# Kernel tuning notes

Measured on AMD Instinct MI355X. Metric: run time of the kernel, lower is better.

The kernel has to match this reference:

```python
import jax, jax.numpy as jnp
import numpy as np

NSEG = 64          # static number of segments (labels in [0, NSEG))
MARGIN = 0.25
W_PUSH = 1.0
W_PULL = 0.1


def setup_inputs() -> dict:
    key = jax.random.key(0)
    k1, k2 = jax.random.split(key)
    preds = jax.random.normal(k1, (4, 2, 16, 512, 512), dtype=jnp.float32)
    labels = jax.random.randint(k2, (4, 1, 512, 512), 0, NSEG, dtype=jnp.int32)
    return {"preds": preds, "labels": labels}


def reference(preds, labels):
    B, S, D, H, W = preds.shape
    P = H * W
    tags = preds.reshape(B, S, D, P)      # [B, n_stack, tag_dim, P]
    seg = labels.reshape(B, P)            # [B, P]
    iu, ju = jnp.triu_indices(NSEG, k=1)  # static upper-triangular pairs

    def per_item(t, s):
        # t: [S, D, P], s: [P]
        # --- scatter-mean: per-segment centroids ---
        tt = t.reshape(S * D, P).T                               # [P, S*D]
        sums = jax.ops.segment_sum(tt, s, num_segments=NSEG)     # [NSEG, S*D]
        counts = jax.ops.segment_sum(jnp.ones((P,), t.dtype), s, num_segments=NSEG)
        cent = (sums / jnp.maximum(counts, 1.0)[:, None]).reshape(NSEG, S, D)
        c = jnp.transpose(cent, (1, 2, 0))                       # [S, D, NSEG]
        # --- push: pairwise L1-mean centroid distance, upper triangle ---
        dist = jnp.abs(c[:, :, :, None] - c[:, :, None, :]).mean(axis=1)  # [S, NSEG, NSEG]
        cd = dist[:, iu, ju]                                     # [S, NSEG*(NSEG-1)/2]
        push = jnp.mean(jax.nn.relu(MARGIN - cd) ** 2)
        # --- pull: gather centroids back to pixels ---
        pc = c[:, :, s]                                          # [S, D, P]
        d = jnp.abs(t - pc).mean(axis=1)                         # [S, P]
        pull = jnp.mean(d ** 2)
        return push, pull

    pushes, pulls = jax.vmap(per_item)(tags, seg)                # [B], [B]
    return (W_PUSH * pushes + W_PULL * pulls).mean()
```

## Files before the change

kernel.cpp:

```cpp
#include <hip/hip_runtime.h>
#include <hip/hip_bf16.h>

#define BB 4
#define SS 2
#define DD 16
#define CH 32
#define PP (512*512)
#define NSEGC 64
#define MARGINF 0.25f
#define CHUNK 1024
#define NCHUNK (PP/CHUNK)

typedef __attribute__((ext_vector_type(4))) float  f32x4;
typedef __attribute__((ext_vector_type(8))) short  short8;

__device__ inline short f2bf(float x) {
    union { __hip_bfloat16 h; short s; } u;
    u.h = __float2bfloat16(x);
    return u.s;
}

__global__ __launch_bounds__(256) void k_sums(const float* __restrict__ preds,
                                              const int* __restrict__ labels,
                                              float* __restrict__ g_sums,
                                              float* __restrict__ g_counts)
{
    __shared__ int   labs[CHUNK];
    __shared__ float buf[4][CH][68];
    __shared__ float cbuf[4][NSEGC];

    const int b    = blockIdx.x / NCHUNK;
    const int base = (blockIdx.x % NCHUNK) * CHUNK;
    const int tid  = threadIdx.x;
    const int w    = tid >> 6;
    const int l    = tid & 63;
    const int lm   = l & 15;
    const int lk   = l >> 4;

    ((int4*)labs)[tid] = ((const int4*)(labels + (size_t)b * PP + base))[tid];

    f32x4 acc[4][2];
    f32x4 accc[4];
#pragma unroll
    for (int mt = 0; mt < 4; ++mt) {
        accc[mt] = f32x4{0.f, 0.f, 0.f, 0.f};
#pragma unroll
        for (int nt = 0; nt < 2; ++nt) acc[mt][nt] = f32x4{0.f, 0.f, 0.f, 0.f};
    }
    short8 ones;
#pragma unroll
    for (int j = 0; j < 8; ++j) ones[j] = (short)0x3F80;

    __syncthreads();

    const float* pb = preds + (size_t)b * CH * PP + base;

#pragma unroll 2
    for (int c = 0; c < 8; ++c) {
        const int kbase = (w * 8 + c) * 32 + lk * 8;
        const int4 L0 = *(const int4*)&labs[kbase];
        const int4 L1 = *(const int4*)&labs[kbase + 4];
        const int labv[8] = {L0.x, L0.y, L0.z, L0.w, L1.x, L1.y, L1.z, L1.w};

        short8 af[4];
#pragma unroll
        for (int mt = 0; mt < 4; ++mt) {
            const int target = mt * 16 + lm;
#pragma unroll
            for (int j = 0; j < 8; ++j)
                af[mt][j] = (labv[j] == target) ? (short)0x3F80 : (short)0;
        }

#pragma unroll
        for (int nt = 0; nt < 2; ++nt) {
            const float* src = pb + (size_t)(nt * 16 + lm) * PP + kbase;
            const float4 v0 = ((const float4*)src)[0];
            const float4 v1 = ((const float4*)src)[1];
            short8 bf;
            bf[0] = f2bf(v0.x); bf[1] = f2bf(v0.y); bf[2] = f2bf(v0.z); bf[3] = f2bf(v0.w);
            bf[4] = f2bf(v1.x); bf[5] = f2bf(v1.y); bf[6] = f2bf(v1.z); bf[7] = f2bf(v1.w);
#pragma unroll
            for (int mt = 0; mt < 4; ++mt)
                acc[mt][nt] = __builtin_amdgcn_mfma_f32_16x16x32_bf16(af[mt], bf, acc[mt][nt], 0, 0, 0);
        }
#pragma unroll
        for (int mt = 0; mt < 4; ++mt)
            accc[mt] = __builtin_amdgcn_mfma_f32_16x16x32_bf16(af[mt], ones, accc[mt], 0, 0, 0);
    }

#pragma unroll
    for (int mt = 0; mt < 4; ++mt) {
#pragma unroll
        for (int nt = 0; nt < 2; ++nt)
            *(f32x4*)&buf[w][nt * 16 + lm][mt * 16 + lk * 4] = acc[mt][nt];
        if (lm == 0)
            *(f32x4*)&cbuf[w][mt * 16 + lk * 4] = accc[mt];
    }
    __syncthreads();

    for (int i = tid; i < CH * NSEGC; i += 256) {
        const int col = i >> 6, row = i & 63;
        const float s = buf[0][col][row] + buf[1][col][row] + buf[2][col][row] + buf[3][col][row];
        atomicAdd(&g_sums[(size_t)b * CH * NSEGC + i], s);
    }
    if (tid < NSEGC)
        atomicAdd(&g_counts[b * NSEGC + tid],
                  cbuf[0][tid] + cbuf[1][tid] + cbuf[2][tid] + cbuf[3][tid]);
}

__global__ __launch_bounds__(256) void k_push(const float* __restrict__ g_sums,
                                              const float* __restrict__ g_counts,
                                              float* __restrict__ g_cent,
                                              float* __restrict__ g_push)
{
    __shared__ float centB[CH * NSEGC];
    __shared__ float red[4];
    const int b = blockIdx.x;
    const int tid = threadIdx.x;

    for (int i = tid; i < CH * NSEGC; i += 256) {
        const int ch = i >> 6, seg = i & 63;
        const float cnt = fmaxf(g_counts[b * NSEGC + seg], 1.0f);
        const float c = g_sums[(size_t)b * CH * NSEGC + i] / cnt;
        centB[i] = c;
        g_cent[(size_t)b * NSEGC * CH + seg * CH + ch] = c;
    }
    __syncthreads();

    float acc = 0.f;
    for (int t = tid; t < SS * 2016; t += 256) {
        const int s = t / 2016;
        int rem = t % 2016;
        int i = 0;
        while (rem >= 63 - i) { rem -= 63 - i; ++i; }
        const int j = i + 1 + rem;
        float dsum = 0.f;
#pragma unroll
        for (int d = 0; d < DD; ++d) {
            const int ch = s * DD + d;
            dsum += fabsf(centB[ch * NSEGC + i] - centB[ch * NSEGC + j]);
        }
        const float cd = dsum * (1.f / DD);
        const float r = fmaxf(MARGINF - cd, 0.f);
        acc += r * r;
    }
    for (int o = 32; o > 0; o >>= 1) acc += __shfl_down(acc, o, 64);
    if ((tid & 63) == 0) red[tid >> 6] = acc;
    __syncthreads();
    if (tid == 0)
        g_push[b] = (red[0] + red[1] + red[2] + red[3]) * (1.0f / (SS * 2016));
}

__global__ __launch_bounds__(256) void k_pull(const float* __restrict__ preds,
                                              const int* __restrict__ labels,
                                              const float* __restrict__ g_cent,
                                              float* __restrict__ g_pull)
{
    __shared__ float centL[NSEGC * 33];
    __shared__ float red[4];
    const int b    = blockIdx.x / NCHUNK;
    const int base = (blockIdx.x % NCHUNK) * CHUNK;
    const int tid  = threadIdx.x;

    for (int i = tid; i < NSEGC * CH; i += 256) {
        const int seg = i >> 5, ch = i & 31;
        centL[seg * 33 + ch] = g_cent[(size_t)b * NSEGC * CH + i];
    }
    const int4 lv = ((const int4*)(labels + (size_t)b * PP + base))[tid];
    const int c0 = lv.x * 33, c1 = lv.y * 33, c2 = lv.z * 33, c3 = lv.w * 33;
    __syncthreads();

    const float* pb = preds + (size_t)b * CH * PP + base;
    float total = 0.f;
#pragma unroll
    for (int s = 0; s < SS; ++s) {
        float a0 = 0.f, a1 = 0.f, a2 = 0.f, a3 = 0.f;
#pragma unroll 8
        for (int d = 0; d < DD; ++d) {
            const int ch = s * DD + d;
            const float4 v = ((const float4*)(pb + (size_t)ch * PP))[tid];
            a0 += fabsf(v.x - centL[c0 + ch]);
            a1 += fabsf(v.y - centL[c1 + ch]);
            a2 += fabsf(v.z - centL[c2 + ch]);
            a3 += fabsf(v.w - centL[c3 + ch]);
        }
        float q;
        q = a0 * (1.f / DD); total += q * q;
        q = a1 * (1.f / DD); total += q * q;
        q = a2 * (1.f / DD); total += q * q;
        q = a3 * (1.f / DD); total += q * q;
    }
    for (int o = 32; o > 0; o >>= 1) total += __shfl_down(total, o, 64);
    if ((tid & 63) == 0) red[tid >> 6] = total;
    __syncthreads();
    if (tid == 0)
        atomicAdd(&g_pull[b], red[0] + red[1] + red[2] + red[3]);
}

__global__ void k_final(const float* __restrict__ g_push,
                        const float* __restrict__ g_pull,
                        float* __restrict__ out)
{
    if (threadIdx.x == 0 && blockIdx.x == 0) {
        float acc = 0.f;
        for (int b = 0; b < BB; ++b)
            acc += g_push[b] + 0.1f * (g_pull[b] * (1.0f / (SS * PP)));
        out[0] = acc * (1.0f / BB);
    }
}

extern "C" void kernel_launch(void* const* d_in, const int* in_sizes, int n_in,
                              void* d_out, int out_size, void* d_ws, size_t ws_size,
                              hipStream_t stream) {
    const float* preds  = (const float*)d_in[0];
    const int*   labels = (const int*)d_in[1];

    float* ws       = (float*)d_ws;
    float* g_sums   = ws;
    float* g_counts = g_sums + BB * CH * NSEGC;
    float* g_pull   = g_counts + BB * NSEGC;
    float* g_push   = g_pull + BB;
    float* g_cent   = g_push + BB;

    hipMemsetAsync(d_ws, 0, (size_t)(BB * CH * NSEGC + BB * NSEGC + BB) * sizeof(float), stream);

    k_sums <<<BB * NCHUNK, 256, 0, stream>>>(preds, labels, g_sums, g_counts);
    k_push <<<BB, 256, 0, stream>>>(g_sums, g_counts, g_cent, g_push);
    k_pull <<<BB * NCHUNK, 256, 0, stream>>>(preds, labels, g_cent, g_pull);
    k_final<<<1, 64, 0, stream>>>(g_push, g_pull, (float*)d_out);
}
```

Baseline: 92.08 us.

## Fuse push and final reduction into pull kernel with last-block finalize

Removes the separate push and final kernels. Each pull block now computes centroids directly from the sums and counts. The first chunk block of each batch also computes the push term, and the last block to finish, detected with an atomic done counter, writes the final scalar. This saves two kernel launches and the serial single-block push kernel. In exchange, every pull block repeats the centroid division, and the push work sits on one block per batch, which may stretch the tail.

Result: slower. 102.2 us (+11.0%).

```diff
diff --git a/kernel.cpp b/kernel.cpp
--- a/kernel.cpp
+++ b/kernel.cpp
@@ -108,55 +108,17 @@
                   cbuf[0][tid] + cbuf[1][tid] + cbuf[2][tid] + cbuf[3][tid]);
 }
 
-__global__ __launch_bounds__(256) void k_push(const float* __restrict__ g_sums,
-                                              const float* __restrict__ g_counts,
-                                              float* __restrict__ g_cent,
-                                              float* __restrict__ g_push)
-{
-    __shared__ float centB[CH * NSEGC];
-    __shared__ float red[4];
-    const int b = blockIdx.x;
-    const int tid = threadIdx.x;
-
-    for (int i = tid; i < CH * NSEGC; i += 256) {
-        const int ch = i >> 6, seg = i & 63;
-        const float cnt = fmaxf(g_counts[b * NSEGC + seg], 1.0f);
-        const float c = g_sums[(size_t)b * CH * NSEGC + i] / cnt;
-        centB[i] = c;
-        g_cent[(size_t)b * NSEGC * CH + seg * CH + ch] = c;
-    }
-    __syncthreads();
-
-    float acc = 0.f;
-    for (int t = tid; t < SS * 2016; t += 256) {
-        const int s = t / 2016;
-        int rem = t % 2016;
-        int i = 0;
-        while (rem >= 63 - i) { rem -= 63 - i; ++i; }
-        const int j = i + 1 + rem;
-        float dsum = 0.f;
-#pragma unroll
-        for (int d = 0; d < DD; ++d) {
-            const int ch = s * DD + d;
-            dsum += fabsf(centB[ch * NSEGC + i] - centB[ch * NSEGC + j]);
-        }
-        const float cd = dsum * (1.f / DD);
-        const float r = fmaxf(MARGINF - cd, 0.f);
-        acc += r * r;
-    }
-    for (int o = 32; o > 0; o >>= 1) acc += __shfl_down(acc, o, 64);
-    if ((tid & 63) == 0) red[tid >> 6] = acc;
-    __syncthreads();
-    if (tid == 0)
-        g_push[b] = (red[0] + red[1] + red[2] + red[3]) * (1.0f / (SS * 2016));
-}
-
-__global__ __launch_bounds__(256) void k_pull(const float* __restrict__ preds,
-                                              const int* __restrict__ labels,
-                                              const float* __restrict__ g_cent,
-                                              float* __restrict__ g_pull)
+__global__ __launch_bounds__(256) void k_pullpush(const float* __restrict__ preds,
+                                                  const int* __restrict__ labels,
+                                                  const float* __restrict__ g_sums,
+                                                  const float* __restrict__ g_counts,
+                                                  float* __restrict__ g_pull,
+                                                  float* __restrict__ g_push,
+                                                  unsigned* __restrict__ g_done,
+                                                  float* __restrict__ out)
 {
     __shared__ float centL[NSEGC * 33];
+    __shared__ float redP[4];
     __shared__ float red[4];
     const int b    = blockIdx.x / NCHUNK;
     const int base = (blockIdx.x % NCHUNK) * CHUNK;
@@ -164,11 +126,37 @@
 
     for (int i = tid; i < NSEGC * CH; i += 256) {
         const int seg = i >> 5, ch = i & 31;
-        centL[seg * 33 + ch] = g_cent[(size_t)b * NSEGC * CH + i];
+        const float cnt = fmaxf(g_counts[b * NSEGC + seg], 1.0f);
+        centL[seg * 33 + ch] = g_sums[(size_t)b * CH * NSEGC + ch * NSEGC + seg] / cnt;
     }
     const int4 lv = ((const int4*)(labels + (size_t)b * PP + base))[tid];
     const int c0 = lv.x * 33, c1 = lv.y * 33, c2 = lv.z * 33, c3 = lv.w * 33;
     __syncthreads();
+
+    if ((blockIdx.x % NCHUNK) == 0) {
+        float acc_p = 0.f;
+        for (int t = tid; t < SS * 2016; t += 256) {
+            const int s = t / 2016;
+            int rem = t % 2016;
+            int i = 0;
+            while (rem >= 63 - i) { rem -= 63 - i; ++i; }
+            const int j = i + 1 + rem;
+            float dsum = 0.f;
+#pragma unroll
+            for (int d = 0; d < DD; ++d) {
+                const int ch = s * DD + d;
+                dsum += fabsf(centL[i * 33 + ch] - centL[j * 33 + ch]);
+            }
+            const float cd = dsum * (1.f / DD);
+            const float r = fmaxf(MARGINF - cd, 0.f);
+            acc_p += r * r;
+        }
+        for (int o = 32; o > 0; o >>= 1) acc_p += __shfl_down(acc_p, o, 64);
+        if ((tid & 63) == 0) redP[tid >> 6] = acc_p;
+        __syncthreads();
+        if (tid == 0)
+            atomicAdd(&g_push[b], (redP[0] + redP[1] + redP[2] + redP[3]) * (1.0f / (SS * 2016)));
+    }
 
     const float* pb = preds + (size_t)b * CH * PP + base;
     float total = 0.f;
@@ -193,19 +181,20 @@
     for (int o = 32; o > 0; o >>= 1) total += __shfl_down(total, o, 64);
     if ((tid & 63) == 0) red[tid >> 6] = total;
     __syncthreads();
-    if (tid == 0)
+
+    if (tid == 0) {
         atomicAdd(&g_pull[b], red[0] + red[1] + red[2] + red[3]);
-}
-
-__global__ void k_final(const float* __restrict__ g_push,
-                        const float* __restrict__ g_pull,
-                        float* __restrict__ out)
-{
-    if (threadIdx.x == 0 && blockIdx.x == 0) {
-        float acc = 0.f;
-        for (int b = 0; b < BB; ++b)
-            acc += g_push[b] + 0.1f * (g_pull[b] * (1.0f / (SS * PP)));
-        out[0] = acc * (1.0f / BB);
+        __threadfence();
+        const unsigned prev = atomicAdd(g_done, 1u);
+        if (prev == gridDim.x - 1) {
+            float accf = 0.f;
+            for (int bb = 0; bb < BB; ++bb) {
+                const float pu = atomicAdd(&g_pull[bb], 0.0f);
+                const float ph = atomicAdd(&g_push[bb], 0.0f);
+                accf += ph + 0.1f * (pu * (1.0f / (SS * PP)));
+            }
+            out[0] = accf * (1.0f / BB);
+        }
     }
 }
 
@@ -220,12 +209,13 @@
     float* g_counts = g_sums + BB * CH * NSEGC;
     float* g_pull   = g_counts + BB * NSEGC;
     float* g_push   = g_pull + BB;
-    float* g_cent   = g_push + BB;
-
-    hipMemsetAsync(d_ws, 0, (size_t)(BB * CH * NSEGC + BB * NSEGC + BB) * sizeof(float), stream);
-
-    k_sums <<<BB * NCHUNK, 256, 0, stream>>>(preds, labels, g_sums, g_counts);
-    k_push <<<BB, 256, 0, stream>>>(g_sums, g_counts, g_cent, g_push);
-    k_pull <<<BB * NCHUNK, 256, 0, stream>>>(preds, labels, g_cent, g_pull);
-    k_final<<<1, 64, 0, stream>>>(g_push, g_pull, (float*)d_out);
-}
+    unsigned* g_done = (unsigned*)(g_push + BB);
+
+    hipMemsetAsync(d_ws, 0,
+                   (size_t)(BB * CH * NSEGC + BB * NSEGC + BB + BB + 1) * sizeof(float),
+                   stream);
+
+    k_sums    <<<BB * NCHUNK, 256, 0, stream>>>(preds, labels, g_sums, g_counts);
+    k_pullpush<<<BB * NCHUNK, 256, 0, stream>>>(preds, labels, g_sums, g_counts,
+                                                g_pull, g_push, g_done, (float*)d_out);
+}
```

## Fuse final reduction into pull kernel and halve pixels per pull block

Applied to the files above, without the earlier changes.

Drops the separate k_final launch. The last pull block to finish, detected through an atomic done-counter, now computes the output. The pull kernel covers 512 pixels per block using float2 loads instead of 1024 with float4, which doubles the grid. It also pads the centroid LDS stride to 36, fully unrolls the channel loop and adds an occupancy hint to launch_bounds. This saves one launch and may improve latency hiding, but narrower loads and twice as many atomics on g_pull could offset the gain.

New measurement: 156.2 us. 1.7x slower.

```diff
diff --git a/kernel.cpp b/kernel.cpp
--- a/kernel.cpp
+++ b/kernel.cpp
@@ -8,8 +8,13 @@
 #define PP (512*512)
 #define NSEGC 64
 #define MARGINF 0.25f
+
 #define CHUNK 1024
 #define NCHUNK (PP/CHUNK)
+
+#define PXB2 512
+#define NCHK2 (PP/PXB2)
+#define CSTR 36
 
 typedef __attribute__((ext_vector_type(4))) float  f32x4;
 typedef __attribute__((ext_vector_type(8))) short  short8;
@@ -151,61 +156,61 @@
         g_push[b] = (red[0] + red[1] + red[2] + red[3]) * (1.0f / (SS * 2016));
 }
 
-__global__ __launch_bounds__(256) void k_pull(const float* __restrict__ preds,
-                                              const int* __restrict__ labels,
-                                              const float* __restrict__ g_cent,
-                                              float* __restrict__ g_pull)
+__global__ __launch_bounds__(256, 6) void k_pull(const float* __restrict__ preds,
+                                                 const int* __restrict__ labels,
+                                                 const float* __restrict__ g_cent,
+                                                 float* __restrict__ g_pull,
+                                                 const float* __restrict__ g_push,
+                                                 unsigned* __restrict__ g_done,
+                                                 float* __restrict__ out)
 {
-    __shared__ float centL[NSEGC * 33];
+    __shared__ float centL[NSEGC * CSTR];
     __shared__ float red[4];
-    const int b    = blockIdx.x / NCHUNK;
-    const int base = (blockIdx.x % NCHUNK) * CHUNK;
+    const int b    = blockIdx.x >> 9;
+    const int base = (blockIdx.x & (NCHK2 - 1)) * PXB2;
     const int tid  = threadIdx.x;
 
     for (int i = tid; i < NSEGC * CH; i += 256) {
         const int seg = i >> 5, ch = i & 31;
-        centL[seg * 33 + ch] = g_cent[(size_t)b * NSEGC * CH + i];
-    }
-    const int4 lv = ((const int4*)(labels + (size_t)b * PP + base))[tid];
-    const int c0 = lv.x * 33, c1 = lv.y * 33, c2 = lv.z * 33, c3 = lv.w * 33;
+        centL[seg * CSTR + ch] = g_cent[(size_t)b * NSEGC * CH + i];
+    }
+    const int2 lv = ((const int2*)(labels + (size_t)b * PP + base))[tid];
+    const int c0 = lv.x * CSTR, c1 = lv.y * CSTR;
     __syncthreads();
 
     const float* pb = preds + (size_t)b * CH * PP + base;
     float total = 0.f;
 #pragma unroll
     for (int s = 0; s < SS; ++s) {
-        float a0 = 0.f, a1 = 0.f, a2 = 0.f, a3 = 0.f;
-#pragma unroll 8
+        float a0 = 0.f, a1 = 0.f;
+#pragma unroll
         for (int d = 0; d < DD; ++d) {
             const int ch = s * DD + d;
-            const float4 v = ((const float4*)(pb + (size_t)ch * PP))[tid];
+            const float2 v = ((const float2*)(pb + (size_t)ch * PP))[tid];
             a0 += fabsf(v.x - centL[c0 + ch]);
             a1 += fabsf(v.y - centL[c1 + ch]);
-            a2 += fabsf(v.z - centL[c2 + ch]);
-            a3 += fabsf(v.w - centL[c3 + ch]);
         }
         float q;
         q = a0 * (1.f / DD); total += q * q;
         q = a1 * (1.f / DD); total += q * q;
-        q = a2 * (1.f / DD); total += q * q;
-        q = a3 * (1.f / DD); total += q * q;
     }
     for (int o = 32; o > 0; o >>= 1) total += __shfl_down(total, o, 64);
     if ((tid & 63) == 0) red[tid >> 6] = total;
     __syncthreads();
-    if (tid == 0)
+
+    if (tid == 0) {
         atomicAdd(&g_pull[b], red[0] + red[1] + red[2] + red[3]);
-}
-
-__global__ void k_final(const float* __restrict__ g_push,
-                        const float* __restrict__ g_pull,
-                        float* __restrict__ out)
-{
-    if (threadIdx.x == 0 && blockIdx.x == 0) {
-        float acc = 0.f;
-        for (int b = 0; b < BB; ++b)
-            acc += g_push[b] + 0.1f * (g_pull[b] * (1.0f / (SS * PP)));
-        out[0] = acc * (1.0f / BB);
+        __threadfence();
+        const unsigned prev = atomicAdd(g_done, 1u);
+        if (prev == gridDim.x - 1) {
+            float accf = 0.f;
+            for (int bb = 0; bb < BB; ++bb) {
+                const float pu = atomicAdd(&g_pull[bb], 0.0f);
+                const float ph = g_push[bb];
+                accf += ph + 0.1f * (pu * (1.0f / (SS * PP)));
+            }
+            out[0] = accf * (1.0f / BB);
+        }
     }
 }
 
@@ -220,12 +225,15 @@
     float* g_counts = g_sums + BB * CH * NSEGC;
     float* g_pull   = g_counts + BB * NSEGC;
     float* g_push   = g_pull + BB;
-    float* g_cent   = g_push + BB;
-
-    hipMemsetAsync(d_ws, 0, (size_t)(BB * CH * NSEGC + BB * NSEGC + BB) * sizeof(float), stream);
-
-    k_sums <<<BB * NCHUNK, 256, 0, stream>>>(preds, labels, g_sums, g_counts);
-    k_push <<<BB, 256, 0, stream>>>(g_sums, g_counts, g_cent, g_push);
-    k_pull <<<BB * NCHUNK, 256, 0, stream>>>(preds, labels, g_cent, g_pull);
-    k_final<<<1, 64, 0, stream>>>(g_push, g_pull, (float*)d_out);
-}
+    unsigned* g_done = (unsigned*)(g_push + BB);
+    float* g_cent   = (float*)(g_done + 1);
+
+    hipMemsetAsync(d_ws, 0,
+                   (size_t)(BB * CH * NSEGC + BB * NSEGC + BB + BB + 1) * sizeof(float),
+                   stream);
+
+    k_sums<<<BB * NCHUNK, 256, 0, stream>>>(preds, labels, g_sums, g_counts);
+    k_push<<<BB, 256, 0, stream>>>(g_sums, g_counts, g_cent, g_push);
+    k_pull<<<BB * NCHK2, 256, 0, stream>>>(preds, labels, g_cent, g_pull, g_push,
+                                           g_done, (float*)d_out);
+}
```
